# Performance work log

Measured on AMD Instinct MI355X. Metric: run time of the kernel, lower is better.

## Reference

```python
import jax, jax.numpy as jnp
import numpy as np

H = 2304; I_FF = 9216; NH = 8; NKV = 4; HD = 256; W = 4096; V = 65536
EPS = 1e-6; SOFTCAP = 30.0; HALF = HD // 2; POS = W // 2  # current decode position
WSCALE = 0.02


def rmsnorm(x, w, eps=EPS):
    return x * jax.lax.rsqrt(jnp.mean(x * x, axis=-1, keepdims=True) + eps) * w


def setup_inputs() -> dict:
    key = jax.random.key(0)
    ks = jax.random.split(key, 16)
    # RoPE angles for position POS
    inv_freq = 1.0 / (10000.0 ** (jnp.arange(HALF, dtype=jnp.float32) / HALF))
    ang = POS * inv_freq
    # attention mask: allow slots <= POS, block the rest
    slot = jnp.arange(W)
    mask = jnp.where(slot <= POS, 0.0, -1e9).astype(jnp.float32).reshape(1, 1, 1, W)
    # one-hot scatter selector for the cache write
    update_idx = jnp.zeros((1, 1, W, 1), jnp.float32).at[0, 0, POS, 0].set(1.0)
    return {
        "hidden_prev": jax.random.normal(ks[0], (1, 1, H), jnp.float32),
        "embed_token": jax.random.normal(ks[1], (1, 1, H), jnp.float32),
        "kv_k_in": jax.random.normal(ks[2], (1, NKV, W, HD), jnp.float32),
        "kv_v_in": jax.random.normal(ks[3], (1, NKV, W, HD), jnp.float32),
        "cos": jnp.cos(ang),
        "sin": jnp.sin(ang),
        "mask": mask,
        "update_idx": update_idx,
        "in_h_w": jax.random.normal(ks[4], (H, H), jnp.float32) * WSCALE,
        "in_e_w": jax.random.normal(ks[5], (H, H), jnp.float32) * WSCALE,
        "input_ln_w": jnp.ones((H,), jnp.float32),
        "post_attn_ln_w": jnp.ones((H,), jnp.float32),
        "pre_ffn_ln_w": jnp.ones((H,), jnp.float32),
        "post_ffn_ln_w": jnp.ones((H,), jnp.float32),
        "final_ln_w": jnp.ones((H,), jnp.float32),
        "q_w": jax.random.normal(ks[6], (NH * HD, H), jnp.float32) * WSCALE,
        "k_w": jax.random.normal(ks[7], (NKV * HD, H), jnp.float32) * WSCALE,
        "v_w": jax.random.normal(ks[8], (NKV * HD, H), jnp.float32) * WSCALE,
        "o_w": jax.random.normal(ks[9], (H, NH * HD), jnp.float32) * WSCALE,
        "q_norm_w": jnp.ones((HD,), jnp.float32),
        "k_norm_w": jnp.ones((HD,), jnp.float32),
        "gate_w": jax.random.normal(ks[10], (I_FF, H), jnp.float32) * WSCALE,
        "up_w": jax.random.normal(ks[11], (I_FF, H), jnp.float32) * WSCALE,
        "down_w": jax.random.normal(ks[12], (H, I_FF), jnp.float32) * WSCALE,
        "lm_head_w": jax.random.normal(ks[13], (V, H), jnp.float32) * WSCALE,
    }


def reference(hidden_prev, embed_token, kv_k_in, kv_v_in, cos, sin, mask, update_idx,
              in_h_w, in_e_w, input_ln_w, post_attn_ln_w, pre_ffn_ln_w, post_ffn_ln_w,
              final_ln_w, q_w, k_w, v_w, o_w, q_norm_w, k_norm_w, gate_w, up_w, down_w,
              lm_head_w):
    # dual input projection (1x1 convs == linear)
    x = hidden_prev @ in_h_w.T + embed_token @ in_e_w.T          # [1,1,H]
    residual = x
    hn = rmsnorm(x, input_ln_w)
    # QKV
    q = (hn @ q_w.T).reshape(1, NH, 1, HD)
    k = (hn @ k_w.T).reshape(1, NKV, 1, HD)
    v = (hn @ v_w.T).reshape(1, NKV, 1, HD)
    q = rmsnorm(q, q_norm_w)
    k = rmsnorm(k, k_norm_w)
    # RoPE (half-split rotation)
    cos_r = cos.reshape(1, 1, 1, HALF)
    sin_r = sin.reshape(1, 1, 1, HALF)
    q1, q2 = q[..., :HALF], q[..., HALF:]
    q = jnp.concatenate([q1 * cos_r - q2 * sin_r, q2 * cos_r + q1 * sin_r], axis=-1)
    k1, k2 = k[..., :HALF], k[..., HALF:]
    k_rot = jnp.concatenate([k1 * cos_r - k2 * sin_r, k2 * cos_r + k1 * sin_r], axis=-1)
    # multiply-based KV cache update
    keep = 1.0 - update_idx                                      # [1,1,W,1]
    kv_k_out = kv_k_in * keep + k_rot * update_idx               # [1,NKV,W,HD]
    kv_v_out = kv_v_in * keep + v * update_idx
    # GQA expansion
    n_rep = NH // NKV
    k_exp = jnp.repeat(kv_k_out, n_rep, axis=1)                  # [1,NH,W,HD]
    v_exp = jnp.repeat(kv_v_out, n_rep, axis=1)
    # fp32 attention
    scale = 1.0 / np.sqrt(HD)
    attn = jnp.einsum('bhqd,bhkd->bhqk', q, k_exp) * scale + mask
    p = jax.nn.softmax(attn, axis=-1)
    out = jnp.einsum('bhqk,bhkd->bhqd', p, v_exp).reshape(1, 1, NH * HD)
    h_attn = rmsnorm(out @ o_w.T, post_attn_ln_w)
    x = residual + h_attn
    residual = x
    # FFN (gelu-gated)
    hf = rmsnorm(x, pre_ffn_ln_w)
    d = (jax.nn.gelu(hf @ gate_w.T, approximate=False) * (hf @ up_w.T)) @ down_w.T
    x = residual + rmsnorm(d, post_ffn_ln_w)
    hidden_out = rmsnorm(x, final_ln_w)
    # lm_head + softcap + argmax
    logits = hidden_out @ lm_head_w.T                            # [1,1,V]
    logits = jnp.tanh(logits / SOFTCAP) * SOFTCAP
    idx = jnp.argmax(logits, axis=-1)                            # [1,1]
    top_k_indices = idx.reshape(1).astype(jnp.int32)
    top_k_values = jnp.take_along_axis(logits, idx[..., None], axis=-1).reshape(1)
    return (top_k_indices, top_k_values, hidden_out, kv_k_out, kv_v_out)
```

## Files before the change

kernel.cpp:

```cpp
#include <hip/hip_runtime.h>
#include <math.h>

#define H      2304
#define I_FF   9216
#define NH     8
#define NKV    4
#define HD     256
#define W_CTX  4096
#define V_SZ   65536
#define POS    2048
#define NCHUNK 16
#define CHUNK  128
#define EPS    1e-6f
#define NBLK_IN   576
#define NBLK_CPY  2048
#define NBLK_LM   4096

enum {
  WS_X    = 0,
  WS_SSQ  = 2304,
  WS_QKV  = 2880,
  WS_ML   = 6976,
  WS_YP   = 7232,
  WS_ATT  = 40000,
  WS_HRAW = 42048,
  WS_X2   = 44352,
  WS_ACT  = 46656,
  WS_DV   = 55872,
  WS_PART = 58176,
  WS_END  = 66368
};

typedef float f4v __attribute__((ext_vector_type(4)));
typedef float f2v __attribute__((ext_vector_type(2)));

__device__ __forceinline__ f4v ntload4(const float* p) {
  return __builtin_nontemporal_load((const f4v*)p);
}
__device__ __forceinline__ float wave_reduce_sum(float v) {
#pragma unroll
  for (int off = 32; off; off >>= 1) v += __shfl_down(v, off);
  return v;
}
__device__ __forceinline__ float dot4(float4 a, float4 b) {
  return a.x * b.x + a.y * b.y + a.z * b.z + a.w * b.w;
}
__device__ __forceinline__ float dot4n(f4v a, float4 b) {
  return a.x * b.x + a.y * b.y + a.z * b.z + a.w * b.w;
}

__global__ void k_input_copy(const float* __restrict__ Wh, const float* __restrict__ We,
                             const float* __restrict__ hprev, const float* __restrict__ emb,
                             float* __restrict__ x, float* __restrict__ ssq_part,
                             const f2v* __restrict__ kin, const f2v* __restrict__ vin,
                             f2v* __restrict__ kout, f2v* __restrict__ vout) {
  int b = blockIdx.x;
  if (b < NBLK_IN) {
    __shared__ float sv[4];
    int wv = threadIdx.x >> 6, lane = threadIdx.x & 63;
    int row = b * 4 + wv;
    const float* wh = Wh + (size_t)row * H;
    const float* we = We + (size_t)row * H;
    const float4* hp = (const float4*)hprev;
    const float4* em = (const float4*)emb;
    float acc = 0.f;
#pragma unroll
    for (int i = 0; i < H / 256; ++i) {
      int idx = lane + i * 64;
      acc += dot4n(ntload4(wh + idx * 4), hp[idx]);
      acc += dot4n(ntload4(we + idx * 4), em[idx]);
    }
    acc = wave_reduce_sum(acc);
    if (lane == 0) { x[row] = acc; sv[wv] = acc * acc; }
    __syncthreads();
    if (threadIdx.x == 0) ssq_part[b] = sv[0] + sv[1] + sv[2] + sv[3];
    return;
  }
  size_t cb = b - NBLK_IN;
  const size_t n = (size_t)NKV * W_CTX * HD / 2;
  for (size_t i = cb * 256 + threadIdx.x; i < n; i += (size_t)NBLK_CPY * 256) {
    __builtin_nontemporal_store(kin[i], kout + i);
    __builtin_nontemporal_store(vin[i], vout + i);
  }
}

__global__ void k_qkv(const float* __restrict__ qw, const float* __restrict__ kw,
                      const float* __restrict__ vw, const float* __restrict__ x,
                      const float* __restrict__ lnw, const float* __restrict__ ssq,
                      float* __restrict__ qkv) {
  __shared__ float red[256];
  int tid = threadIdx.x;
  float s = ssq[tid] + ssq[tid + 256] + (tid < 64 ? ssq[tid + 512] : 0.f);
  red[tid] = s; __syncthreads();
  for (int st = 128; st; st >>= 1) { if (tid < st) red[tid] += red[tid + st]; __syncthreads(); }
  float scale = rsqrtf(red[0] / (float)H + EPS);

  int row  = (blockIdx.x * 256 + tid) >> 6;
  int lane = tid & 63;
  const float* Wrow;
  if (row < 2048)      Wrow = qw + (size_t)row * H;
  else if (row < 3072) Wrow = kw + (size_t)(row - 2048) * H;
  else                 Wrow = vw + (size_t)(row - 3072) * H;
  const float4* xv = (const float4*)x;
  const float4* l4 = (const float4*)lnw;
  float acc = 0.f;
#pragma unroll
  for (int i = 0; i < H / 256; ++i) {
    int idx = lane + i * 64;
    f4v w = ntload4(Wrow + idx * 4);
    float4 hx = xv[idx], wl = l4[idx];
    acc += w.x * (hx.x * scale * wl.x) + w.y * (hx.y * scale * wl.y) +
           w.z * (hx.z * scale * wl.z) + w.w * (hx.w * scale * wl.w);
  }
  acc = wave_reduce_sum(acc);
  if (lane == 0) qkv[row] = acc;
}

__global__ void k_attn(const float* __restrict__ qkv, const float* __restrict__ qnw,
                       const float* __restrict__ knw, const float* __restrict__ cosv,
                       const float* __restrict__ sinv, const float* __restrict__ kin,
                       const float* __restrict__ vin, float* __restrict__ kv_k_out,
                       float* __restrict__ kv_v_out, float* __restrict__ ml,
                       float* __restrict__ ypart) {
  int h = blockIdx.x >> 4, j = blockIdx.x & 15, kvh = h >> 1;
  int tid = threadIdx.x, lane = tid & 63, wv = tid >> 6;
  __shared__ float qs[HD], ks[HD], sc[CHUNK + 1], red[256];
  float qv = qkv[h * HD + tid];
  float kv = qkv[2048 + kvh * HD + tid];
  red[tid] = qv * qv; __syncthreads();
  for (int s = 128; s; s >>= 1) { if (tid < s) red[tid] += red[tid + s]; __syncthreads(); }
  float sq = rsqrtf(red[0] / (float)HD + EPS);
  __syncthreads();
  red[tid] = kv * kv; __syncthreads();
  for (int s = 128; s; s >>= 1) { if (tid < s) red[tid] += red[tid + s]; __syncthreads(); }
  float sk = rsqrtf(red[0] / (float)HD + EPS);
  qs[tid] = qv * sq * qnw[tid];
  ks[tid] = kv * sk * knw[tid];
  __syncthreads();
  if (tid < HD / 2) {
    float c = cosv[tid], s2 = sinv[tid];
    float q1 = qs[tid], q2 = qs[tid + 128];
    qs[tid] = q1 * c - q2 * s2;  qs[tid + 128] = q2 * c + q1 * s2;
    float k1 = ks[tid], k2 = ks[tid + 128];
    ks[tid] = k1 * c - k2 * s2;  ks[tid + 128] = k2 * c + k1 * s2;
  }
  __syncthreads();
  if (j == 0 && (h & 1) == 0) {
    kv_k_out[((size_t)kvh * W_CTX + POS) * HD + tid] = ks[tid];
    kv_v_out[((size_t)kvh * W_CTX + POS) * HD + tid] = qkv[3072 + kvh * HD + tid];
  }
  int base = j * CHUNK;
  int clen = (j == NCHUNK - 1) ? CHUNK + 1 : CHUNK;
  float4 qf = ((const float4*)qs)[lane];
  const float4* Kb = (const float4*)(kin + ((size_t)kvh * W_CTX + base) * HD);
  for (int i = wv; i < clen; i += 4) {
    float4 kk = (i < CHUNK) ? Kb[(size_t)i * (HD / 4) + lane] : ((const float4*)ks)[lane];
    float acc = dot4(qf, kk);
    acc = wave_reduce_sum(acc);
    if (lane == 0) sc[i] = acc * 0.0625f;
  }
  __syncthreads();
  float m = -1e30f;
  for (int i = tid; i < clen; i += 256) m = fmaxf(m, sc[i]);
  red[tid] = m; __syncthreads();
  for (int s = 128; s; s >>= 1) { if (tid < s) red[tid] = fmaxf(red[tid], red[tid + s]); __syncthreads(); }
  m = red[0]; __syncthreads();
  float ss = 0.f;
  for (int i = tid; i < clen; i += 256) { float e = expf(sc[i] - m); sc[i] = e; ss += e; }
  red[tid] = ss; __syncthreads();
  for (int s = 128; s; s >>= 1) { if (tid < s) red[tid] += red[tid + s]; __syncthreads(); }
  if (tid == 0) { ml[(h * NCHUNK + j) * 2] = m; ml[(h * NCHUNK + j) * 2 + 1] = red[0]; }
  __syncthreads();
  const float* Vb = vin + ((size_t)kvh * W_CTX + base) * HD;
  float a0 = 0.f, a1 = 0.f, a2 = 0.f, a3 = 0.f;
  for (int s = 0; s < CHUNK; s += 4) {
    a0 += sc[s]     * Vb[(size_t)s * HD + tid];
    a1 += sc[s + 1] * Vb[(size_t)(s + 1) * HD + tid];
    a2 += sc[s + 2] * Vb[(size_t)(s + 2) * HD + tid];
    a3 += sc[s + 3] * Vb[(size_t)(s + 3) * HD + tid];
  }
  if (clen > CHUNK) a0 += sc[CHUNK] * qkv[3072 + kvh * HD + tid];
  ypart[(size_t)(h * NCHUNK + j) * HD + tid] = a0 + a1 + a2 + a3;
}

__global__ void k_attn_comb(const float* __restrict__ ml, const float* __restrict__ ypart,
                            float* __restrict__ att) {
  int h = blockIdx.x, tid = threadIdx.x;
  float M = -1e30f;
#pragma unroll
  for (int j = 0; j < NCHUNK; ++j) M = fmaxf(M, ml[(h * NCHUNK + j) * 2]);
  float L = 0.f, acc = 0.f;
#pragma unroll
  for (int j = 0; j < NCHUNK; ++j) {
    float w = expf(ml[(h * NCHUNK + j) * 2] - M);
    L += ml[(h * NCHUNK + j) * 2 + 1] * w;
    acc += ypart[(size_t)(h * NCHUNK + j) * HD + tid] * w;
  }
  att[h * HD + tid] = acc / L;
}

template <int NCOLS>
__global__ void k_gemv_t(const float* __restrict__ Wm, const float* __restrict__ x,
                         float* __restrict__ y) {
  int row  = (blockIdx.x * 256 + threadIdx.x) >> 6;
  int lane = threadIdx.x & 63;
  const float* wr = Wm + (size_t)row * NCOLS;
  const float4* xv = (const float4*)x;
  float acc = 0.f;
#pragma unroll 4
  for (int i = 0; i < NCOLS / 256; ++i) {
    int idx = lane + i * 64;
    acc += dot4n(ntload4(wr + idx * 4), xv[idx]);
  }
  acc = wave_reduce_sum(acc);
  if (lane == 0) y[row] = acc;
}

__global__ void k_gateup(const float* __restrict__ gw, const float* __restrict__ uw,
                         const float* __restrict__ x, const float* __restrict__ hraw,
                         const float* __restrict__ w_post, const float* __restrict__ w_pre,
                         float* __restrict__ x2_out, float* __restrict__ act) {
  __shared__ float red[256];
  __shared__ float hfs[H];
  int tid = threadIdx.x;
  float lh[9], lx2[9];
  float ss = 0.f;
#pragma unroll
  for (int k = 0; k < 9; ++k) { lh[k] = hraw[tid + k * 256]; ss += lh[k] * lh[k]; }
  red[tid] = ss; __syncthreads();
  for (int s = 128; s; s >>= 1) { if (tid < s) red[tid] += red[tid + s]; __syncthreads(); }
  float sc1 = rsqrtf(red[0] / (float)H + EPS);
  __syncthreads();
  float ss2 = 0.f;
#pragma unroll
  for (int k = 0; k < 9; ++k) {
    int i = tid + k * 256;
    float v = x[i] + lh[k] * sc1 * w_post[i];
    lx2[k] = v; ss2 += v * v;
  }
  red[tid] = ss2; __syncthreads();
  for (int s = 128; s; s >>= 1) { if (tid < s) red[tid] += red[tid + s]; __syncthreads(); }
  float sc2 = rsqrtf(red[0] / (float)H + EPS);
#pragma unroll
  for (int k = 0; k < 9; ++k) { int i = tid + k * 256; hfs[i] = lx2[k] * sc2 * w_pre[i]; }
  if (blockIdx.x == 0) {
#pragma unroll
    for (int k = 0; k < 9; ++k) { int i = tid + k * 256; x2_out[i] = lx2[k]; }
  }
  __syncthreads();
  int row  = (blockIdx.x * 256 + tid) >> 6;
  int lane = tid & 63;
  const float* g4 = gw + (size_t)row * H;
  const float* u4 = uw + (size_t)row * H;
  const float4* h4 = (const float4*)hfs;
  float ag = 0.f, au = 0.f;
#pragma unroll
  for (int i = 0; i < H / 256; ++i) {
    int idx = lane + i * 64;
    float4 hh = h4[idx];
    ag += dot4n(ntload4(g4 + idx * 4), hh);
    au += dot4n(ntload4(u4 + idx * 4), hh);
  }
  ag = wave_reduce_sum(ag);
  au = wave_reduce_sum(au);
  if (lane == 0) {
    float gl = 0.5f * ag * (1.f + erff(ag * 0.70710678118f));
    act[row] = gl * au;
  }
}

__global__ void k_lmhead(const float* __restrict__ Wm, const float* __restrict__ x2,
                         const float* __restrict__ dv, const float* __restrict__ w_post,
                         const float* __restrict__ w_fin, float* __restrict__ hid_out,
                         float2* __restrict__ partials) {
  __shared__ float red[256];
  __shared__ float hid[H];
  __shared__ float bv[4]; __shared__ int bi[4];
  int tid = threadIdx.x;
  float ld[9], lx3[9];
  float ss = 0.f;
#pragma unroll
  for (int k = 0; k < 9; ++k) { ld[k] = dv[tid + k * 256]; ss += ld[k] * ld[k]; }
  red[tid] = ss; __syncthreads();
  for (int s = 128; s; s >>= 1) { if (tid < s) red[tid] += red[tid + s]; __syncthreads(); }
  float sc1 = rsqrtf(red[0] / (float)H + EPS);
  __syncthreads();
  float ss2 = 0.f;
#pragma unroll
  for (int k = 0; k < 9; ++k) {
    int i = tid + k * 256;
    float v = x2[i] + ld[k] * sc1 * w_post[i];
    lx3[k] = v; ss2 += v * v;
  }
  red[tid] = ss2; __syncthreads();
  for (int s = 128; s; s >>= 1) { if (tid < s) red[tid] += red[tid + s]; __syncthreads(); }
  float sc2 = rsqrtf(red[0] / (float)H + EPS);
#pragma unroll
  for (int k = 0; k < 9; ++k) { int i = tid + k * 256; hid[i] = lx3[k] * sc2 * w_fin[i]; }
  if (blockIdx.x == 0) {
#pragma unroll
    for (int k = 0; k < 9; ++k) { int i = tid + k * 256; hid_out[i] = hid[i]; }
  }
  __syncthreads();
  int gw   = (blockIdx.x * 256 + tid) >> 6;
  int lane = tid & 63;
  int wv   = tid >> 6;
  const float4* hv = (const float4*)hid;
  int row0 = gw * 4;
  const float* w0 = Wm + (size_t)(row0 + 0) * H;
  const float* w1 = Wm + (size_t)(row0 + 1) * H;
  const float* w2 = Wm + (size_t)(row0 + 2) * H;
  const float* w3 = Wm + (size_t)(row0 + 3) * H;
  float a0 = 0.f, a1 = 0.f, a2 = 0.f, a3 = 0.f;
#pragma unroll
  for (int i = 0; i < H / 256; ++i) {
    int idx = lane + i * 64;
    float4 b = hv[idx];
    a0 += dot4n(ntload4(w0 + idx * 4), b);
    a1 += dot4n(ntload4(w1 + idx * 4), b);
    a2 += dot4n(ntload4(w2 + idx * 4), b);
    a3 += dot4n(ntload4(w3 + idx * 4), b);
  }
  a0 = wave_reduce_sum(a0);
  a1 = wave_reduce_sum(a1);
  a2 = wave_reduce_sum(a2);
  a3 = wave_reduce_sum(a3);
  if (lane == 0) {
    float l0 = 30.f * tanhf(a0 * (1.f / 30.f));
    float l1 = 30.f * tanhf(a1 * (1.f / 30.f));
    float l2 = 30.f * tanhf(a2 * (1.f / 30.f));
    float l3 = 30.f * tanhf(a3 * (1.f / 30.f));
    float best = l0; int bidx = row0;
    if (l1 > best) { best = l1; bidx = row0 + 1; }
    if (l2 > best) { best = l2; bidx = row0 + 2; }
    if (l3 > best) { best = l3; bidx = row0 + 3; }
    bv[wv] = best; bi[wv] = bidx;
  }
  __syncthreads();
  if (tid == 0) {
    float B = bv[0]; int I = bi[0];
    for (int i = 1; i < 4; ++i)
      if (bv[i] > B || (bv[i] == B && bi[i] < I)) { B = bv[i]; I = bi[i]; }
    partials[blockIdx.x] = make_float2(B, (float)I);
  }
}

__global__ void k_argmax_final(const float2* __restrict__ partials, int n,
                               float* __restrict__ out) {
  __shared__ float bv[256]; __shared__ int bi[256];
  int tid = threadIdx.x;
  float best = -1e30f; int bidx = 0x7fffffff;
  for (int i = tid; i < n; i += 256) {
    float2 p = partials[i];
    int pi = (int)p.y;
    if (p.x > best || (p.x == best && pi < bidx)) { best = p.x; bidx = pi; }
  }
  bv[tid] = best; bi[tid] = bidx; __syncthreads();
  for (int s = 128; s; s >>= 1) {
    if (tid < s) {
      if (bv[tid + s] > bv[tid] || (bv[tid + s] == bv[tid] && bi[tid + s] < bi[tid])) {
        bv[tid] = bv[tid + s]; bi[tid] = bi[tid + s];
      }
    }
    __syncthreads();
  }
  if (tid == 0) { out[0] = (float)bi[0]; out[1] = bv[0]; }
}

extern "C" void kernel_launch(void* const* d_in, const int* in_sizes, int n_in,
                              void* d_out, int out_size, void* d_ws, size_t ws_size,
                              hipStream_t stream) {
  const float* hidden_prev = (const float*)d_in[0];
  const float* embed_token = (const float*)d_in[1];
  const float* kv_k_in     = (const float*)d_in[2];
  const float* kv_v_in     = (const float*)d_in[3];
  const float* cosv        = (const float*)d_in[4];
  const float* sinv        = (const float*)d_in[5];
  const float* in_h_w      = (const float*)d_in[8];
  const float* in_e_w      = (const float*)d_in[9];
  const float* input_ln_w  = (const float*)d_in[10];
  const float* post_attn_w = (const float*)d_in[11];
  const float* pre_ffn_w   = (const float*)d_in[12];
  const float* post_ffn_w  = (const float*)d_in[13];
  const float* final_ln_w  = (const float*)d_in[14];
  const float* q_w         = (const float*)d_in[15];
  const float* k_w         = (const float*)d_in[16];
  const float* v_w         = (const float*)d_in[17];
  const float* o_w         = (const float*)d_in[18];
  const float* q_norm_w    = (const float*)d_in[19];
  const float* k_norm_w    = (const float*)d_in[20];
  const float* gate_w      = (const float*)d_in[21];
  const float* up_w        = (const float*)d_in[22];
  const float* down_w      = (const float*)d_in[23];
  const float* lm_head_w   = (const float*)d_in[24];

  float* out     = (float*)d_out;
  float* out_hid = out + 2;
  float* out_kvk = out + 2 + H;
  float* out_kvv = out_kvk + (size_t)NKV * W_CTX * HD;
  float* ws      = (float*)d_ws;

  k_input_copy<<<NBLK_IN + NBLK_CPY, 256, 0, stream>>>(
      in_h_w, in_e_w, hidden_prev, embed_token, ws + WS_X, ws + WS_SSQ,
      (const f2v*)kv_k_in, (const f2v*)kv_v_in, (f2v*)out_kvk, (f2v*)out_kvv);
  k_qkv<<<1024, 256, 0, stream>>>(q_w, k_w, v_w, ws + WS_X, input_ln_w,
                                  ws + WS_SSQ, ws + WS_QKV);
  k_attn<<<NH * NCHUNK, 256, 0, stream>>>(ws + WS_QKV, q_norm_w, k_norm_w, cosv, sinv,
                                          kv_k_in, kv_v_in, out_kvk, out_kvv,
                                          ws + WS_ML, ws + WS_YP);
  k_attn_comb<<<NH, 256, 0, stream>>>(ws + WS_ML, ws + WS_YP, ws + WS_ATT);
  k_gemv_t<NH * HD><<<H / 4, 256, 0, stream>>>(o_w, ws + WS_ATT, ws + WS_HRAW);
  k_gateup<<<I_FF / 4, 256, 0, stream>>>(gate_w, up_w, ws + WS_X, ws + WS_HRAW,
                                         post_attn_w, pre_ffn_w, ws + WS_X2, ws + WS_ACT);
  k_gemv_t<I_FF><<<H / 4, 256, 0, stream>>>(down_w, ws + WS_ACT, ws + WS_DV);
  k_lmhead<<<NBLK_LM, 256, 0, stream>>>(lm_head_w, ws + WS_X2, ws + WS_DV,
                                        post_ffn_w, final_ln_w, out_hid,
                                        (float2*)(ws + WS_PART));
  k_argmax_final<<<1, 256, 0, stream>>>((const float2*)(ws + WS_PART), NBLK_LM, out);

  (void)in_sizes; (void)n_in; (void)out_size; (void)ws_size;
}
```

Before: 227.0 us.

## Move KV cache copy into attention kernel, fuse attn combine into o-proj

Moves the KV cache copy out of the input-projection kernel and into extra blocks of the attention kernel, skipping the POS slot that attention writes. It halves the attention chunk size so there are more attention blocks, and folds the split-softmax combine into the o_proj GEMV kernel, with every block recomputing the combine. Shared-memory tree reductions are replaced with wave shuffles plus a 4-entry shared reduction. The intent is to overlap the bandwidth-heavy copy with attention and to cut launches and barriers. In exchange, the combine work is duplicated across 576 blocks, and the copy now competes with attention for memory bandwidth.

```diff
diff --git a/kernel.cpp b/kernel.cpp
--- a/kernel.cpp
+++ b/kernel.cpp
@@ -9,11 +9,12 @@
 #define W_CTX  4096
 #define V_SZ   65536
 #define POS    2048
-#define NCHUNK 16
-#define CHUNK  128
+#define NCHUNK 32
+#define CHUNK  64
+#define NATTN  (NH * NCHUNK)
+#define NBLK_ATTN_TOTAL 2048
 #define EPS    1e-6f
 #define NBLK_IN   576
-#define NBLK_CPY  2048
 #define NBLK_LM   4096
 
 enum {
@@ -21,14 +22,13 @@
   WS_SSQ  = 2304,
   WS_QKV  = 2880,
   WS_ML   = 6976,
-  WS_YP   = 7232,
-  WS_ATT  = 40000,
-  WS_HRAW = 42048,
-  WS_X2   = 44352,
-  WS_ACT  = 46656,
-  WS_DV   = 55872,
-  WS_PART = 58176,
-  WS_END  = 66368
+  WS_YP   = 7488,
+  WS_HRAW = 73024,
+  WS_X2   = 75328,
+  WS_ACT  = 77632,
+  WS_DV   = 86848,
+  WS_PART = 89152,
+  WS_END  = 97344
 };
 
 typedef float f4v __attribute__((ext_vector_type(4)));
@@ -42,6 +42,11 @@
   for (int off = 32; off; off >>= 1) v += __shfl_down(v, off);
   return v;
 }
+__device__ __forceinline__ float wave_reduce_max(float v) {
+#pragma unroll
+  for (int off = 32; off; off >>= 1) v = fmaxf(v, __shfl_down(v, off));
+  return v;
+}
 __device__ __forceinline__ float dot4(float4 a, float4 b) {
   return a.x * b.x + a.y * b.y + a.z * b.z + a.w * b.w;
 }
@@ -49,54 +54,42 @@
   return a.x * b.x + a.y * b.y + a.z * b.z + a.w * b.w;
 }
 
-__global__ void k_input_copy(const float* __restrict__ Wh, const float* __restrict__ We,
-                             const float* __restrict__ hprev, const float* __restrict__ emb,
-                             float* __restrict__ x, float* __restrict__ ssq_part,
-                             const f2v* __restrict__ kin, const f2v* __restrict__ vin,
-                             f2v* __restrict__ kout, f2v* __restrict__ vout) {
-  int b = blockIdx.x;
-  if (b < NBLK_IN) {
-    __shared__ float sv[4];
-    int wv = threadIdx.x >> 6, lane = threadIdx.x & 63;
-    int row = b * 4 + wv;
-    const float* wh = Wh + (size_t)row * H;
-    const float* we = We + (size_t)row * H;
-    const float4* hp = (const float4*)hprev;
-    const float4* em = (const float4*)emb;
-    float acc = 0.f;
-#pragma unroll
-    for (int i = 0; i < H / 256; ++i) {
-      int idx = lane + i * 64;
-      acc += dot4n(ntload4(wh + idx * 4), hp[idx]);
-      acc += dot4n(ntload4(we + idx * 4), em[idx]);
-    }
-    acc = wave_reduce_sum(acc);
-    if (lane == 0) { x[row] = acc; sv[wv] = acc * acc; }
-    __syncthreads();
-    if (threadIdx.x == 0) ssq_part[b] = sv[0] + sv[1] + sv[2] + sv[3];
-    return;
-  }
-  size_t cb = b - NBLK_IN;
-  const size_t n = (size_t)NKV * W_CTX * HD / 2;
-  for (size_t i = cb * 256 + threadIdx.x; i < n; i += (size_t)NBLK_CPY * 256) {
-    __builtin_nontemporal_store(kin[i], kout + i);
-    __builtin_nontemporal_store(vin[i], vout + i);
-  }
+__global__ void k_input(const float* __restrict__ Wh, const float* __restrict__ We,
+                        const float* __restrict__ hprev, const float* __restrict__ emb,
+                        float* __restrict__ x, float* __restrict__ ssq_part) {
+  __shared__ float sv[4];
+  int wv = threadIdx.x >> 6, lane = threadIdx.x & 63;
+  int row = blockIdx.x * 4 + wv;
+  const float* wh = Wh + (size_t)row * H;
+  const float* we = We + (size_t)row * H;
+  const float4* hp = (const float4*)hprev;
+  const float4* em = (const float4*)emb;
+  float acc = 0.f;
+#pragma unroll
+  for (int i = 0; i < H / 256; ++i) {
+    int idx = lane + i * 64;
+    acc += dot4n(ntload4(wh + idx * 4), hp[idx]);
+    acc += dot4n(ntload4(we + idx * 4), em[idx]);
+  }
+  acc = wave_reduce_sum(acc);
+  if (lane == 0) { x[row] = acc; sv[wv] = acc * acc; }
+  __syncthreads();
+  if (threadIdx.x == 0) ssq_part[blockIdx.x] = sv[0] + sv[1] + sv[2] + sv[3];
 }
 
 __global__ void k_qkv(const float* __restrict__ qw, const float* __restrict__ kw,
                       const float* __restrict__ vw, const float* __restrict__ x,
                       const float* __restrict__ lnw, const float* __restrict__ ssq,
                       float* __restrict__ qkv) {
-  __shared__ float red[256];
-  int tid = threadIdx.x;
+  __shared__ float sred[4];
+  int tid = threadIdx.x, lane = tid & 63, wv = tid >> 6;
   float s = ssq[tid] + ssq[tid + 256] + (tid < 64 ? ssq[tid + 512] : 0.f);
-  red[tid] = s; __syncthreads();
-  for (int st = 128; st; st >>= 1) { if (tid < st) red[tid] += red[tid + st]; __syncthreads(); }
-  float scale = rsqrtf(red[0] / (float)H + EPS);
-
-  int row  = (blockIdx.x * 256 + tid) >> 6;
-  int lane = tid & 63;
+  s = wave_reduce_sum(s);
+  if (lane == 0) sred[wv] = s;
+  __syncthreads();
+  float scale = rsqrtf((sred[0] + sred[1] + sred[2] + sred[3]) / (float)H + EPS);
+
+  int row = (blockIdx.x * 256 + tid) >> 6;
   const float* Wrow;
   if (row < 2048)      Wrow = qw + (size_t)row * H;
   else if (row < 3072) Wrow = kw + (size_t)(row - 2048) * H;
@@ -121,19 +114,35 @@
                        const float* __restrict__ sinv, const float* __restrict__ kin,
                        const float* __restrict__ vin, float* __restrict__ kv_k_out,
                        float* __restrict__ kv_v_out, float* __restrict__ ml,
-                       float* __restrict__ ypart) {
-  int h = blockIdx.x >> 4, j = blockIdx.x & 15, kvh = h >> 1;
+                       float* __restrict__ ypart,
+                       const f2v* __restrict__ kin2, const f2v* __restrict__ vin2,
+                       f2v* __restrict__ kout2, f2v* __restrict__ vout2) {
+  int b = blockIdx.x;
   int tid = threadIdx.x, lane = tid & 63, wv = tid >> 6;
-  __shared__ float qs[HD], ks[HD], sc[CHUNK + 1], red[256];
+  if (b >= NATTN) {
+    size_t cb = b - NATTN;
+    const size_t n = (size_t)NKV * W_CTX * HD / 2;
+    const size_t stride = (size_t)(NBLK_ATTN_TOTAL - NATTN) * 256;
+    for (size_t i = cb * 256 + tid; i < n; i += stride) {
+      int slot = (int)((i >> 7) & (W_CTX - 1));
+      if (slot != POS) {
+        __builtin_nontemporal_store(kin2[i], kout2 + i);
+        __builtin_nontemporal_store(vin2[i], vout2 + i);
+      }
+    }
+    return;
+  }
+  int h = b >> 5, j = b & 31, kvh = h >> 1;
+  __shared__ float qs[HD], ks[HD], sc[CHUNK + 1];
+  __shared__ float sredq[4], sredk[4];
   float qv = qkv[h * HD + tid];
   float kv = qkv[2048 + kvh * HD + tid];
-  red[tid] = qv * qv; __syncthreads();
-  for (int s = 128; s; s >>= 1) { if (tid < s) red[tid] += red[tid + s]; __syncthreads(); }
-  float sq = rsqrtf(red[0] / (float)HD + EPS);
-  __syncthreads();
-  red[tid] = kv * kv; __syncthreads();
-  for (int s = 128; s; s >>= 1) { if (tid < s) red[tid] += red[tid + s]; __syncthreads(); }
-  float sk = rsqrtf(red[0] / (float)HD + EPS);
+  float pq = wave_reduce_sum(qv * qv);
+  float pk = wave_reduce_sum(kv * kv);
+  if (lane == 0) { sredq[wv] = pq; sredk[wv] = pk; }
+  __syncthreads();
+  float sq = rsqrtf((sredq[0] + sredq[1] + sredq[2] + sredq[3]) / (float)HD + EPS);
+  float sk = rsqrtf((sredk[0] + sredk[1] + sredk[2] + sredk[3]) / (float)HD + EPS);
   qs[tid] = qv * sq * qnw[tid];
   ks[tid] = kv * sk * knw[tid];
   __syncthreads();
@@ -162,15 +171,19 @@
   __syncthreads();
   float m = -1e30f;
   for (int i = tid; i < clen; i += 256) m = fmaxf(m, sc[i]);
-  red[tid] = m; __syncthreads();
-  for (int s = 128; s; s >>= 1) { if (tid < s) red[tid] = fmaxf(red[tid], red[tid + s]); __syncthreads(); }
-  m = red[0]; __syncthreads();
-  float ss = 0.f;
-  for (int i = tid; i < clen; i += 256) { float e = expf(sc[i] - m); sc[i] = e; ss += e; }
-  red[tid] = ss; __syncthreads();
-  for (int s = 128; s; s >>= 1) { if (tid < s) red[tid] += red[tid + s]; __syncthreads(); }
-  if (tid == 0) { ml[(h * NCHUNK + j) * 2] = m; ml[(h * NCHUNK + j) * 2 + 1] = red[0]; }
-  __syncthreads();
+  m = wave_reduce_max(m);
+  if (lane == 0) sredq[wv] = m;
+  __syncthreads();
+  float M = fmaxf(fmaxf(sredq[0], sredq[1]), fmaxf(sredq[2], sredq[3]));
+  float ssum = 0.f;
+  for (int i = tid; i < clen; i += 256) { float e = expf(sc[i] - M); sc[i] = e; ssum += e; }
+  ssum = wave_reduce_sum(ssum);
+  if (lane == 0) sredk[wv] = ssum;
+  __syncthreads();
+  if (tid == 0) {
+    ml[(h * NCHUNK + j) * 2]     = M;
+    ml[(h * NCHUNK + j) * 2 + 1] = sredk[0] + sredk[1] + sredk[2] + sredk[3];
+  }
   const float* Vb = vin + ((size_t)kvh * W_CTX + base) * HD;
   float a0 = 0.f, a1 = 0.f, a2 = 0.f, a3 = 0.f;
   for (int s = 0; s < CHUNK; s += 4) {
@@ -183,54 +196,63 @@
   ypart[(size_t)(h * NCHUNK + j) * HD + tid] = a0 + a1 + a2 + a3;
 }
 
-__global__ void k_attn_comb(const float* __restrict__ ml, const float* __restrict__ ypart,
-                            float* __restrict__ att) {
-  int h = blockIdx.x, tid = threadIdx.x;
+__global__ void k_o(const float* __restrict__ ow, const float* __restrict__ ml,
+                    const float* __restrict__ yp, float* __restrict__ hraw) {
+  __shared__ float lmm[256], lml[256], ew[256], Lh[8];
+  __shared__ float atts[NH * HD];
+  int tid = threadIdx.x, lane = tid & 63, wv = tid >> 6;
+  lmm[tid] = ml[2 * tid];
+  lml[tid] = ml[2 * tid + 1];
+  __syncthreads();
+  int hh = tid >> 5;
   float M = -1e30f;
-#pragma unroll
-  for (int j = 0; j < NCHUNK; ++j) M = fmaxf(M, ml[(h * NCHUNK + j) * 2]);
-  float L = 0.f, acc = 0.f;
-#pragma unroll
-  for (int j = 0; j < NCHUNK; ++j) {
-    float w = expf(ml[(h * NCHUNK + j) * 2] - M);
-    L += ml[(h * NCHUNK + j) * 2 + 1] * w;
-    acc += ypart[(size_t)(h * NCHUNK + j) * HD + tid] * w;
-  }
-  att[h * HD + tid] = acc / L;
-}
-
-template <int NCOLS>
-__global__ void k_gemv_t(const float* __restrict__ Wm, const float* __restrict__ x,
-                         float* __restrict__ y) {
-  int row  = (blockIdx.x * 256 + threadIdx.x) >> 6;
-  int lane = threadIdx.x & 63;
-  const float* wr = Wm + (size_t)row * NCOLS;
-  const float4* xv = (const float4*)x;
+#pragma unroll 8
+  for (int jj = 0; jj < 32; ++jj) M = fmaxf(M, lmm[hh * 32 + jj]);
+  ew[tid] = expf(lmm[tid] - M);
+  __syncthreads();
+  if ((tid & 31) == 0) {
+    float L = 0.f;
+#pragma unroll 8
+    for (int jj = 0; jj < 32; ++jj) L += lml[tid + jj] * ew[tid + jj];
+    Lh[tid >> 5] = L;
+  }
+  __syncthreads();
+  for (int h2 = 0; h2 < 8; ++h2) {
+    float acc = 0.f;
+#pragma unroll 8
+    for (int jj = 0; jj < 32; ++jj)
+      acc += ew[h2 * 32 + jj] * yp[(size_t)(h2 * 32 + jj) * HD + tid];
+    atts[h2 * HD + tid] = acc / Lh[h2];
+  }
+  __syncthreads();
+  int row = blockIdx.x * 4 + wv;
+  const float* wr = ow + (size_t)row * (NH * HD);
+  const float4* xv = (const float4*)atts;
   float acc = 0.f;
-#pragma unroll 4
-  for (int i = 0; i < NCOLS / 256; ++i) {
+#pragma unroll
+  for (int i = 0; i < (NH * HD) / 256; ++i) {
     int idx = lane + i * 64;
     acc += dot4n(ntload4(wr + idx * 4), xv[idx]);
   }
   acc = wave_reduce_sum(acc);
-  if (lane == 0) y[row] = acc;
+  if (lane == 0) hraw[row] = acc;
 }
 
 __global__ void k_gateup(const float* __restrict__ gw, const float* __restrict__ uw,
                          const float* __restrict__ x, const float* __restrict__ hraw,
                          const float* __restrict__ w_post, const float* __restrict__ w_pre,
                          float* __restrict__ x2_out, float* __restrict__ act) {
-  __shared__ float red[256];
   __shared__ float hfs[H];
-  int tid = threadIdx.x;
+  __shared__ float srA[4], srB[4];
+  int tid = threadIdx.x, lane = tid & 63, wv = tid >> 6;
   float lh[9], lx2[9];
   float ss = 0.f;
 #pragma unroll
   for (int k = 0; k < 9; ++k) { lh[k] = hraw[tid + k * 256]; ss += lh[k] * lh[k]; }
-  red[tid] = ss; __syncthreads();
-  for (int s = 128; s; s >>= 1) { if (tid < s) red[tid] += red[tid + s]; __syncthreads(); }
-  float sc1 = rsqrtf(red[0] / (float)H + EPS);
-  __syncthreads();
+  ss = wave_reduce_sum(ss);
+  if (lane == 0) srA[wv] = ss;
+  __syncthreads();
+  float sc1 = rsqrtf((srA[0] + srA[1] + srA[2] + srA[3]) / (float)H + EPS);
   float ss2 = 0.f;
 #pragma unroll
   for (int k = 0; k < 9; ++k) {
@@ -238,9 +260,10 @@
     float v = x[i] + lh[k] * sc1 * w_post[i];
     lx2[k] = v; ss2 += v * v;
   }
-  red[tid] = ss2; __syncthreads();
-  for (int s = 128; s; s >>= 1) { if (tid < s) red[tid] += red[tid + s]; __syncthreads(); }
-  float sc2 = rsqrtf(red[0] / (float)H + EPS);
+  ss2 = wave_reduce_sum(ss2);
+  if (lane == 0) srB[wv] = ss2;
+  __syncthreads();
+  float sc2 = rsqrtf((srB[0] + srB[1] + srB[2] + srB[3]) / (float)H + EPS);
 #pragma unroll
   for (int k = 0; k < 9; ++k) { int i = tid + k * 256; hfs[i] = lx2[k] * sc2 * w_pre[i]; }
   if (blockIdx.x == 0) {
@@ -248,8 +271,7 @@
     for (int k = 0; k < 9; ++k) { int i = tid + k * 256; x2_out[i] = lx2[k]; }
   }
   __syncthreads();
-  int row  = (blockIdx.x * 256 + tid) >> 6;
-  int lane = tid & 63;
+  int row = (blockIdx.x * 256 + tid) >> 6;
   const float* g4 = gw + (size_t)row * H;
   const float* u4 = uw + (size_t)row * H;
   const float4* h4 = (const float4*)hfs;
@@ -257,9 +279,9 @@
 #pragma unroll
   for (int i = 0; i < H / 256; ++i) {
     int idx = lane + i * 64;
-    float4 hh = h4[idx];
-    ag += dot4n(ntload4(g4 + idx * 4), hh);
-    au += dot4n(ntload4(u4 + idx * 4), hh);
+    float4 hh2 = h4[idx];
+    ag += dot4n(ntload4(g4 + idx * 4), hh2);
+    au += dot4n(ntload4(u4 + idx * 4), hh2);
   }
   ag = wave_reduce_sum(ag);
   au = wave_reduce_sum(au);
@@ -269,22 +291,38 @@
   }
 }
 
+__global__ void k_down(const float* __restrict__ dw, const float* __restrict__ actv,
+                       float* __restrict__ dv) {
+  int row  = (blockIdx.x * 256 + threadIdx.x) >> 6;
+  int lane = threadIdx.x & 63;
+  const float* wr = dw + (size_t)row * I_FF;
+  const float4* xv = (const float4*)actv;
+  float acc = 0.f;
+#pragma unroll 4
+  for (int i = 0; i < I_FF / 256; ++i) {
+    int idx = lane + i * 64;
+    acc += dot4n(ntload4(wr + idx * 4), xv[idx]);
+  }
+  acc = wave_reduce_sum(acc);
+  if (lane == 0) dv[row] = acc;
+}
+
 __global__ void k_lmhead(const float* __restrict__ Wm, const float* __restrict__ x2,
                          const float* __restrict__ dv, const float* __restrict__ w_post,
                          const float* __restrict__ w_fin, float* __restrict__ hid_out,
                          float2* __restrict__ partials) {
-  __shared__ float red[256];
   __shared__ float hid[H];
+  __shared__ float srA[4], srB[4];
   __shared__ float bv[4]; __shared__ int bi[4];
-  int tid = threadIdx.x;
+  int tid = threadIdx.x, lane = tid & 63, wv = tid >> 6;
   float ld[9], lx3[9];
   float ss = 0.f;
 #pragma unroll
   for (int k = 0; k < 9; ++k) { ld[k] = dv[tid + k * 256]; ss += ld[k] * ld[k]; }
-  red[tid] = ss; __syncthreads();
-  for (int s = 128; s; s >>= 1) { if (tid < s) red[tid] += red[tid + s]; __syncthreads(); }
-  float sc1 = rsqrtf(red[0] / (float)H + EPS);
-  __syncthreads();
+  ss = wave_reduce_sum(ss);
+  if (lane == 0) srA[wv] = ss;
+  __syncthreads();
+  float sc1 = rsqrtf((srA[0] + srA[1] + srA[2] + srA[3]) / (float)H + EPS);
   float ss2 = 0.f;
 #pragma unroll
   for (int k = 0; k < 9; ++k) {
@@ -292,9 +330,10 @@
     float v = x2[i] + ld[k] * sc1 * w_post[i];
     lx3[k] = v; ss2 += v * v;
   }
-  red[tid] = ss2; __syncthreads();
-  for (int s = 128; s; s >>= 1) { if (tid < s) red[tid] += red[tid + s]; __syncthreads(); }
-  float sc2 = rsqrtf(red[0] / (float)H + EPS);
+  ss2 = wave_reduce_sum(ss2);
+  if (lane == 0) srB[wv] = ss2;
+  __syncthreads();
+  float sc2 = rsqrtf((srB[0] + srB[1] + srB[2] + srB[3]) / (float)H + EPS);
 #pragma unroll
   for (int k = 0; k < 9; ++k) { int i = tid + k * 256; hid[i] = lx3[k] * sc2 * w_fin[i]; }
   if (blockIdx.x == 0) {
@@ -303,8 +342,6 @@
   }
   __syncthreads();
   int gw   = (blockIdx.x * 256 + tid) >> 6;
-  int lane = tid & 63;
-  int wv   = tid >> 6;
   const float4* hv = (const float4*)hid;
   int row0 = gw * 4;
   const float* w0 = Wm + (size_t)(row0 + 0) * H;
@@ -400,19 +437,18 @@
   float* out_kvv = out_kvk + (size_t)NKV * W_CTX * HD;
   float* ws      = (float*)d_ws;
 
-  k_input_copy<<<NBLK_IN + NBLK_CPY, 256, 0, stream>>>(
-      in_h_w, in_e_w, hidden_prev, embed_token, ws + WS_X, ws + WS_SSQ,
-      (const f2v*)kv_k_in, (const f2v*)kv_v_in, (f2v*)out_kvk, (f2v*)out_kvv);
+  k_input<<<NBLK_IN, 256, 0, stream>>>(in_h_w, in_e_w, hidden_prev, embed_token,
+                                       ws + WS_X, ws + WS_SSQ);
   k_qkv<<<1024, 256, 0, stream>>>(q_w, k_w, v_w, ws + WS_X, input_ln_w,
                                   ws + WS_SSQ, ws + WS_QKV);
-  k_attn<<<NH * NCHUNK, 256, 0, stream>>>(ws + WS_QKV, q_norm_w, k_norm_w, cosv, sinv,
-                                          kv_k_in, kv_v_in, out_kvk, out_kvv,
-                                          ws + WS_ML, ws + WS_YP);
-  k_attn_comb<<<NH, 256, 0, stream>>>(ws + WS_ML, ws + WS_YP, ws + WS_ATT);
-  k_gemv_t<NH * HD><<<H / 4, 256, 0, stream>>>(o_w, ws + WS_ATT, ws + WS_HRAW);
+  k_attn<<<NBLK_ATTN_TOTAL, 256, 0, stream>>>(
+      ws + WS_QKV, q_norm_w, k_norm_w, cosv, sinv, kv_k_in, kv_v_in,
+      out_kvk, out_kvv, ws + WS_ML, ws + WS_YP,
+      (const f2v*)kv_k_in, (const f2v*)kv_v_in, (f2v*)out_kvk, (f2v*)out_kvv);
+  k_o<<<H / 4, 256, 0, stream>>>(o_w, ws + WS_ML, ws + WS_YP, ws + WS_HRAW);
   k_gateup<<<I_FF / 4, 256, 0, stream>>>(gate_w, up_w, ws + WS_X, ws + WS_HRAW,
                                          post_attn_w, pre_ffn_w, ws + WS_X2, ws + WS_ACT);
-  k_gemv_t<I_FF><<<H / 4, 256, 0, stream>>>(down_w, ws + WS_ACT, ws + WS_DV);
+  k_down<<<H / 4, 256, 0, stream>>>(down_w, ws + WS_ACT, ws + WS_DV);
   k_lmhead<<<NBLK_LM, 256, 0, stream>>>(lm_head_w, ws + WS_X2, ws + WS_DV,
                                         post_ffn_w, final_ln_w, out_hid,
                                         (float2*)(ws + WS_PART));
```

New measurement: 205.1 us. 1.11x faster.
